# Kernel optimization log

Hardware: AMD Instinct MI355X
Metric: run time of the kernel (lower is better)

## Reference

```python
import jax, jax.numpy as jnp
import numpy as np
import math

K, D_FEAT, L_FAC, N = 128, 1024, 16, 16384


def setup_inputs() -> dict:
    key = jax.random.key(0)
    k1, k2, k3, k4 = jax.random.split(key, 4)
    x = jax.random.normal(k1, (N, D_FEAT), dtype=jnp.float32)
    MU = 0.1 * jax.random.normal(k2, (K, D_FEAT), dtype=jnp.float32)
    A = 0.05 * jax.random.normal(k3, (K, D_FEAT, L_FAC), dtype=jnp.float32)
    # D must be positive (it is a per-feature noise std): uniform in [0.1, 0.5]
    D = jax.random.uniform(k4, (K, D_FEAT), dtype=jnp.float32, minval=0.1, maxval=0.5)
    PI = jnp.ones((K,), dtype=jnp.float32) / K
    return {"x": x, "PI": PI, "MU": MU, "A": A, "D": D}


def reference(x, PI, MU, A, D):
    # Faithful vectorized version of MFA._per_component_log_likelihood.
    k, d, l = A.shape
    iD = jnp.power(D, -2.0)                      # (K, d)  = 1/D^2
    iDA = iD[:, :, None] * A                     # (K, d, l)
    # Woodbury small matrix: L = I_l + A^T (iD * A)
    Lm = jnp.eye(l, dtype=A.dtype)[None] + jnp.einsum('kdl,kdm->klm', A, iDA)
    iL = jnp.linalg.inv(Lm)                      # (K, l, l)

    # y[k,n,:] = A^T (iD * (x_n - MU_k))  without materializing (K,N,d)
    y = jnp.einsum('nd,kdl->knl', x, iDA) - jnp.einsum('kd,kdl->kl', MU, iDA)[:, None, :]
    # term1[k,n] = sum_d iD[k,d] * (x_n - MU_k)^2, expanded to avoid (K,N,d)
    term1 = (jnp.einsum('nd,kd->kn', x * x, iD)
             - 2.0 * jnp.einsum('nd,kd->kn', x, iD * MU)
             + jnp.sum(iD * MU * MU, axis=1)[:, None])
    # quadratic correction: y^T iL y
    quad = jnp.einsum('knl,klm,knm->kn', y, iL, y)
    m_d = term1 - quad                           # (K, N) Mahalanobis distances

    det_L = jnp.linalg.slogdet(Lm)[1]            # (K,)
    log_det_Sigma = det_L - jnp.sum(jnp.log(iD), axis=1)
    log2pi = jnp.asarray(math.log(2.0 * math.pi), dtype=x.dtype)
    log_prob = -0.5 * ((d * log2pi + log_det_Sigma)[:, None] + m_d)  # (K, N)
    # NOTE: original adds raw PI (not log PI) -- replicated faithfully.
    return PI[None, :] + log_prob.T              # (N, K)
```

## Files before the change

### kernel.cpp

```cpp
#include <hip/hip_runtime.h>
#include <math.h>

typedef unsigned short ushort_t;
typedef unsigned char  uchar_t;
typedef __attribute__((ext_vector_type(8))) short short8v;
typedef __attribute__((ext_vector_type(4))) float f32x4;
typedef __attribute__((ext_vector_type(2))) long l64x2;

#define KCOMP 128
#define DF    1024
#define LF    16
#define NPTS  16384
#define LOG2PI 1.8378770664093453f

#define XQ_OFF    ((size_t)0)
#define XQ_BYTES  ((size_t)NPTS*DF)
#define BQ_OFF    (XQ_OFF + XQ_BYTES)
#define BQ_BYTES  ((size_t)2048*DF)
#define BSK_OFF   (BQ_OFF + BQ_BYTES)
#define BSK_BYTES ((size_t)KCOMP*2*DF*2)
#define CSK_OFF   (BSK_OFF + BSK_BYTES)
#define FULL_NEED (CSK_OFF + 512)

__device__ __forceinline__ ushort_t f2bf(float f) {
  union { float f; unsigned u; } v; v.f = f;
  unsigned u = v.u;
  return (ushort_t)((u + 0x7FFFu + ((u >> 16) & 1u)) >> 16);
}

#define GLOAD16(gp, lp) __builtin_amdgcn_global_load_lds( \
  (const __attribute__((address_space(1))) unsigned int*)(gp), \
  (__attribute__((address_space(3))) unsigned int*)(lp), 16, 0, 0)

#define DPPADD(x, ctrl) do { \
  int _yi = __builtin_amdgcn_update_dpp(0, __float_as_int(x), ctrl, 0xF, 0xF, true); \
  (x) += __int_as_float(_yi); } while (0)

__global__ __launch_bounds__(256) void mfa_pre(
    const float* __restrict__ PI, const float* __restrict__ MU,
    const float* __restrict__ A, const float* __restrict__ Dm,
    uchar_t* __restrict__ Bq, ushort_t* __restrict__ Bsk,
    float* __restrict__ csk)
{
  const int k = blockIdx.x, t = threadIdx.x;
  const int tl = t >> 4, tm = t & 15;
  __shared__ float As[64][16];
  __shared__ float iD64[64], MU64[64];
  __shared__ float R[16][17];
  __shared__ float rinv_s[16], zsh[16], bsh[16];
  __shared__ float red[64];
  __shared__ float sc_sumlog, sc_c3;

  float accL = 0.f, accb = 0.f, c3p = 0.f, slogp = 0.f;
  for (int ch = 0; ch < 16; ++ch) {
    __syncthreads();
    ((float4*)&As[0][0])[t] =
        ((const float4*)(A + (size_t)k*DF*LF + (size_t)ch*1024))[t];
    if (t < 64) {
      float dv = Dm[k*DF + ch*64 + t];
      iD64[t] = 1.f/(dv*dv);
      MU64[t] = MU[k*DF + ch*64 + t];
    }
    __syncthreads();
    #pragma unroll 4
    for (int dd = 0; dd < 64; ++dd)
      accL = fmaf(As[dd][tl]*iD64[dd], As[dd][tm], accL);
    if (tm == 0)
      for (int dd = 0; dd < 64; ++dd)
        accb = fmaf(iD64[dd]*MU64[dd], As[dd][tl], accb);
    if (t < 64) {
      c3p = fmaf(iD64[t]*MU64[t], MU64[t], c3p);
      slogp += logf(iD64[t]);
    }
  }
  __syncthreads();
  R[tl][tm] = accL + (tl == tm ? 1.f : 0.f);
  if (tm == 0) bsh[tl] = accb;
  if (t < 64) red[t] = slogp;
  __syncthreads();
  if (t == 0) { float s = 0.f; for (int i = 0; i < 64; ++i) s += red[i]; sc_sumlog = s; }
  __syncthreads();
  if (t < 64) red[t] = c3p;
  __syncthreads();
  if (t == 0) { float s = 0.f; for (int i = 0; i < 64; ++i) s += red[i]; sc_c3 = s; }

  for (int j = 0; j < 16; ++j) {
    __syncthreads();
    if (t == j) {
      float s = R[j][j];
      for (int i = 0; i < j; ++i) s -= R[j][i]*R[j][i];
      float rj = sqrtf(s);
      R[j][j] = rj; rinv_s[j] = 1.f/rj;
    }
    __syncthreads();
    if (t < 16 && t > j) {
      float s = R[t][j];
      for (int i = 0; i < j; ++i) s -= R[t][i]*R[j][i];
      R[t][j] = s * rinv_s[j];
    }
  }
  __syncthreads();
  if (t == 0) {
    float ldet = 0.f;
    for (int j = 0; j < 16; ++j) ldet += 2.f*logf(R[j][j]);
    float w[16], z[16];
    for (int j = 0; j < 16; ++j) {
      float s = bsh[j];
      for (int i = 0; i < j; ++i) s -= R[j][i]*w[i];
      w[j] = s*rinv_s[j];
    }
    for (int j = 15; j >= 0; --j) {
      float s = w[j];
      for (int i = j+1; i < 16; ++i) s -= R[i][j]*z[i];
      z[j] = s*rinv_s[j];
      zsh[j] = z[j];
    }
    float muh = sc_c3;
    for (int l = 0; l < 16; ++l) muh -= bsh[l]*zsh[l];
    csk[k] = PI[k] - 0.5f*((float)DF*LOG2PI + ldet - sc_sumlog) - 0.5f*muh;
  }
  __syncthreads();

  for (int it = 0; it < 4; ++it) {
    const int d = t + it*256;
    float dv = Dm[k*DF + d];
    float iD = 1.f/(dv*dv);
    float mu = MU[k*DF + d];
    float v[16], gg[16];
    #pragma unroll
    for (int l = 0; l < 16; ++l) v[l] = iD * A[((size_t)k*DF + d)*LF + l];
    #pragma unroll
    for (int j = 0; j < 16; ++j) {
      float s = v[j];
      #pragma unroll
      for (int i = 0; i < 16; ++i) if (i < j) s -= R[j][i]*gg[i];
      gg[j] = s * rinv_s[j];
    }
    float h = iD*mu;
    #pragma unroll
    for (int l = 0; l < 16; ++l) h -= v[l]*zsh[l];
    const int dd = d & 63;
    const size_t poff = (size_t)(d & ~63) + ((dd >> 3) & 3)*16 + (dd >> 5)*8 + (dd & 7);
    #pragma unroll
    for (int l = 0; l < 16; ++l) {
      int r8 = __builtin_amdgcn_cvt_pk_fp8_f32(gg[l], gg[l], 0, false);
      Bq[(size_t)(k*16 + l)*DF + poff] = (uchar_t)(r8 & 0xFF);
    }
    Bsk[(size_t)k*2*DF + d]      = f2bf(-2.f*h);
    Bsk[(size_t)k*2*DF + DF + d] = f2bf(iD);
  }
}

__global__ __launch_bounds__(256) void mfa_sk2q(
    const float* __restrict__ x, const ushort_t* __restrict__ Bsk,
    const float* __restrict__ csk, uchar_t* __restrict__ xq,
    float* __restrict__ out)
{
  __shared__ ushort_t xs[4096];
  __shared__ ushort_t x2s[4096];
  __shared__ ushort_t Bs[16384];
  const int t = threadIdx.x, lane = t & 63, wid = t >> 6;
  const int wc = wid;
  const int lr = lane & 15, lh = lane >> 4;
  const int n0 = blockIdx.x * 64;
  const int xr = t >> 2, xc = t & 3;

  f32x4 acc[4][2] = {};

  float4 v0, v1, v2, v3;
  {
    const float* xp = x + (size_t)(n0 + xr)*DF + xc*16;
    v0 = ((const float4*)xp)[0]; v1 = ((const float4*)xp)[1];
    v2 = ((const float4*)xp)[2]; v3 = ((const float4*)xp)[3];
  }

  for (int tt = 0; tt < 16; ++tt) {
    const int d0 = tt * 64;
    __syncthreads();
    {
      float e[16] = {v0.x,v0.y,v0.z,v0.w, v1.x,v1.y,v1.z,v1.w,
                     v2.x,v2.y,v2.z,v2.w, v3.x,v3.y,v3.z,v3.w};
      short8v b0, b1, q0, q1;
      #pragma unroll
      for (int i = 0; i < 8; ++i) {
        b0[i] = (short)f2bf(e[i]);     q0[i] = (short)f2bf(e[i]*e[i]);
        b1[i] = (short)f2bf(e[8+i]);   q1[i] = (short)f2bf(e[8+i]*e[8+i]);
      }
      const int ch0 = (xc*2) ^ (xr & 7), ch1 = (xc*2+1) ^ (xr & 7);
      *(short8v*)&xs[xr*64 + ch0*8]  = b0;
      *(short8v*)&xs[xr*64 + ch1*8]  = b1;
      *(short8v*)&x2s[xr*64 + ch0*8] = q0;
      *(short8v*)&x2s[xr*64 + ch1*8] = q1;
      int p0 = 0, p1 = 0, p2 = 0, p3 = 0;
      p0 = __builtin_amdgcn_cvt_pk_fp8_f32(e[0],  e[1],  p0, false);
      p0 = __builtin_amdgcn_cvt_pk_fp8_f32(e[2],  e[3],  p0, true);
      p1 = __builtin_amdgcn_cvt_pk_fp8_f32(e[4],  e[5],  p1, false);
      p1 = __builtin_amdgcn_cvt_pk_fp8_f32(e[6],  e[7],  p1, true);
      p2 = __builtin_amdgcn_cvt_pk_fp8_f32(e[8],  e[9],  p2, false);
      p2 = __builtin_amdgcn_cvt_pk_fp8_f32(e[10], e[11], p2, true);
      p3 = __builtin_amdgcn_cvt_pk_fp8_f32(e[12], e[13], p3, false);
      p3 = __builtin_amdgcn_cvt_pk_fp8_f32(e[14], e[15], p3, true);
      long lo = (long)(((unsigned long long)(unsigned)p1 << 32) | (unsigned)p0);
      long hi = (long)(((unsigned long long)(unsigned)p3 << 32) | (unsigned)p2);
      size_t base = (size_t)(n0 + xr)*DF + d0 + (xc & 1)*32 + (xc >> 1)*8;
      *(long*)&xq[base]      = lo;
      *(long*)&xq[base + 16] = hi;
    }
    #pragma unroll
    for (int j = 0; j < 8; ++j) {
      int v = (wid*8 + j)*8 + (lane >> 3);
      int g = (lane & 7) ^ (v & 7);
      const ushort_t* src = (v < 128)
        ? Bsk + (size_t)v*(2*DF) + d0 + g*8
        : Bsk + (size_t)(v - 128)*(2*DF) + DF + d0 + g*8;
      GLOAD16(src, (char*)Bs + (wid*8 + j)*1024);
    }
    __syncthreads();
    if (tt < 15) {
      const float* xp = x + (size_t)(n0 + xr)*DF + (d0 + 64) + xc*16;
      v0 = ((const float4*)xp)[0]; v1 = ((const float4*)xp)[1];
      v2 = ((const float4*)xp)[2]; v3 = ((const float4*)xp)[3];
    }
    __builtin_amdgcn_sched_barrier(0);
    #pragma unroll
    for (int ks = 0; ks < 2; ++ks) {
      const int cterm = ((ks*4 + lh) ^ (lr & 7)) * 8;
      short8v a_[4], a2_[4], bh[2], bi[2];
      #pragma unroll
      for (int rb = 0; rb < 4; ++rb) {
        a_[rb]  = *(const short8v*)&xs[(rb*16 + lr)*64 + cterm];
        a2_[rb] = *(const short8v*)&x2s[(rb*16 + lr)*64 + cterm];
      }
      #pragma unroll
      for (int cb = 0; cb < 2; ++cb) {
        int vh = wc*32 + cb*16 + lr;
        bh[cb] = *(const short8v*)&Bs[vh*64 + cterm];
        bi[cb] = *(const short8v*)&Bs[(128 + vh)*64 + cterm];
      }
      #pragma unroll
      for (int cb = 0; cb < 2; ++cb)
        #pragma unroll
        for (int rb = 0; rb < 4; ++rb) {
          acc[rb][cb] = __builtin_amdgcn_mfma_f32_16x16x32_bf16(a_[rb],  bh[cb], acc[rb][cb], 0,0,0);
          acc[rb][cb] = __builtin_amdgcn_mfma_f32_16x16x32_bf16(a2_[rb], bi[cb], acc[rb][cb], 0,0,0);
        }
    }
  }
  #pragma unroll
  for (int cb = 0; cb < 2; ++cb) {
    int comp = wc*32 + cb*16 + lr;
    float ck = csk[comp];
    #pragma unroll
    for (int rb = 0; rb < 4; ++rb)
      #pragma unroll
      for (int j = 0; j < 4; ++j) {
        int row = n0 + rb*16 + lh*4 + j;
        out[(size_t)row*KCOMP + comp] = ck - 0.5f*acc[rb][cb][j];
      }
  }
}

__global__ __launch_bounds__(1024, 4) void mfa_gemm8(
    const uchar_t* __restrict__ xq, const uchar_t* __restrict__ Bq,
    float* __restrict__ out)
{
  __shared__ uchar_t smem[65536];
  const int t = threadIdx.x, lane = t & 63, wid = t >> 6;
  const int wm = wid & 3, wn = wid >> 2;
  const int lr = lane & 15, lh = lane >> 4;

  const int bid = blockIdx.x;
  const int xcd = bid & 7, ib = bid >> 3;
  const int rb = xcd*8 + (ib >> 3);
  const int cb = ib & 7;
  const int n0 = rb * 256, c0 = cb * 256;

  f32x4 acc[4][4] = {};

  const int js = (((lane & 3) ^ ((lane >> 3) & 3)) * 16);
  const uchar_t* srcP[2]; int dstO[2];
  #pragma unroll
  for (int q = 0; q < 2; ++q) {
    int id = wid*2 + q;
    if (id < 16) {
      int r = id*16 + (lane >> 2);
      srcP[q] = xq + (size_t)(n0 + r)*DF + js;
      dstO[q] = id*1024 + (lane & 3)*16 + (lane >> 2)*64 - (lane)*16;
    } else {
      int cr = (id - 16)*16 + (lane >> 2);
      srcP[q] = Bq + (size_t)(c0 + cr)*DF + js;
    }
  }
  dstO[0] = (wid*2 + 0) < 16 ? (wid*2+0)*1024 : 16384 + ((wid*2+0)-16)*1024;
  dstO[1] = (wid*2 + 1) < 16 ? (wid*2+1)*1024 : 16384 + ((wid*2+1)-16)*1024;

  const int rsw = (lh ^ ((lr >> 1) & 3)) * 16;
  const int aO = (wm*64 + lr)*64 + rsw;
  const int bO = 16384 + (wn*64 + lr)*64 + rsw;

  #define STAGE8(slot, tt_) do { \
    _Pragma("unroll") \
    for (int q = 0; q < 2; ++q) \
      GLOAD16(srcP[q] + (tt_)*64, (char*)smem + (slot)*32768 + dstO[q] + (lane & 63)*0 + ((lane)*16 & 1023)); \
  } while (0)

  STAGE8(0, 0);
  STAGE8(1, 1);

  for (int tt = 0; tt < 16; ++tt) {
    const char* lb = (const char*)smem + (tt & 1)*32768;
    l64x2 a2[4], b2[4];

    if (tt < 15) asm volatile("s_waitcnt vmcnt(2)" ::: "memory");
    else         asm volatile("s_waitcnt vmcnt(0)" ::: "memory");
    __builtin_amdgcn_s_barrier();

    #pragma unroll
    for (int rt = 0; rt < 4; ++rt) a2[rt] = *(const l64x2*)(lb + aO + rt*1024);
    #pragma unroll
    for (int ct = 0; ct < 4; ++ct) b2[ct] = *(const l64x2*)(lb + bO + ct*1024);
    asm volatile("s_waitcnt lgkmcnt(0)" ::: "memory");
    __builtin_amdgcn_sched_barrier(0);
    __builtin_amdgcn_s_barrier();
    if (tt <= 13) STAGE8(tt & 1, tt + 2);
    __builtin_amdgcn_sched_barrier(0);

    __builtin_amdgcn_s_setprio(1);
    #pragma unroll
    for (int ct = 0; ct < 4; ++ct)
      #pragma unroll
      for (int rt = 0; rt < 4; ++rt)
        acc[rt][ct] = __builtin_amdgcn_mfma_f32_16x16x32_fp8_fp8(a2[rt][0], b2[ct][0], acc[rt][ct], 0,0,0);
    #pragma unroll
    for (int ct = 0; ct < 4; ++ct)
      #pragma unroll
      for (int rt = 0; rt < 4; ++rt)
        acc[rt][ct] = __builtin_amdgcn_mfma_f32_16x16x32_fp8_fp8(a2[rt][1], b2[ct][1], acc[rt][ct], 0,0,0);
    __builtin_amdgcn_s_setprio(0);
  }

  #pragma unroll
  for (int ct = 0; ct < 4; ++ct) {
    const int comp = cb*16 + wn*4 + ct;
    #pragma unroll
    for (int rt = 0; rt < 4; ++rt) {
      #pragma unroll
      for (int j = 0; j < 4; ++j) {
        float v = acc[rt][ct][j];
        float sq = v*v;
        DPPADD(sq, 0xB1);
        DPPADD(sq, 0x4E);
        DPPADD(sq, 0x124);
        DPPADD(sq, 0x128);
        if (lr == 0) {
          int row = n0 + wm*64 + rt*16 + lh*4 + j;
          size_t idx = (size_t)row * KCOMP + comp;
          out[idx] = out[idx] + 0.5f*sq;
        }
      }
    }
  }
}

#define FB_NG 8
#define FB_CG 288
#define FB_BN 128
#define FB_DT 32
#define FB_PITCH 40
#define FB_BMAT_ELEMS ((size_t)(FB_NG*FB_CG)*DF)
#define FB_CST_OFF (FB_BMAT_ELEMS*2)
#define FB_MUH_OFF (FB_CST_OFF + 512)

__global__ __launch_bounds__(256) void fb_pre(
    const float* __restrict__ PI, const float* __restrict__ MU,
    const float* __restrict__ A, const float* __restrict__ Dm,
    ushort_t* __restrict__ Bmat, float* __restrict__ cst, float* __restrict__ muh)
{
  const int k = blockIdx.x, t = threadIdx.x;
  const int tl = t >> 4, tm = t & 15;
  __shared__ float As[16][16], iDsh[16], MUsh[16];
  __shared__ float R[16][17], rinv[16], zsh[16], bsh[16];
  __shared__ float red[256];

  float accL = 0.f, accb = 0.f, slog = 0.f;
  for (int d0 = 0; d0 < DF; d0 += 16) {
    __syncthreads();
    As[tl][tm] = A[((size_t)k*DF + d0 + tl)*LF + tm];
    if (t < 16) {
      float dv = Dm[k*DF + d0 + t];
      iDsh[t] = 1.f/(dv*dv);
      MUsh[t] = MU[k*DF + d0 + t];
    }
    __syncthreads();
    #pragma unroll
    for (int dd = 0; dd < 16; ++dd)
      accL = fmaf(As[dd][tl]*iDsh[dd], As[dd][tm], accL);
    if (tm == 0) {
      #pragma unroll
      for (int dd = 0; dd < 16; ++dd)
        accb = fmaf(iDsh[dd]*MUsh[dd], As[dd][tl], accb);
    }
    if (t < 16) slog += logf(iDsh[t]);
  }
  __syncthreads();
  R[tl][tm] = accL + (tl == tm ? 1.f : 0.f);
  if (tm == 0) bsh[tl] = accb;
  red[t] = (t < 16) ? slog : 0.f;
  __syncthreads();
  float sumlogiD = 0.f;
  if (t == 0) { for (int i = 0; i < 16; ++i) sumlogiD += red[i]; }

  for (int j = 0; j < 16; ++j) {
    if (t == j) {
      float s = R[j][j];
      for (int i = 0; i < j; ++i) s -= R[j][i]*R[j][i];
      float rj = sqrtf(s);
      R[j][j] = rj; rinv[j] = 1.f/rj;
    }
    __syncthreads();
    if (t < 16 && t > j) {
      float s = R[t][j];
      for (int i = 0; i < j; ++i) s -= R[t][i]*R[j][i];
      R[t][j] = s * rinv[j];
    }
    __syncthreads();
  }

  float ldet = 0.f;
  if (t == 0) {
    #pragma unroll
    for (int j = 0; j < 16; ++j) ldet += 2.f*logf(R[j][j]);
    float w[16], z[16];
    #pragma unroll
    for (int j = 0; j < 16; ++j) {
      float s = bsh[j];
      #pragma unroll
      for (int i = 0; i < 16; ++i) if (i < j) s -= R[j][i]*w[i];
      w[j] = s*rinv[j];
    }
    #pragma unroll
    for (int j = 15; j >= 0; --j) {
      float s = w[j];
      #pragma unroll
      for (int i = 0; i < 16; ++i) if (i > j) s -= R[i][j]*z[i];
      z[j] = s*rinv[j];
      zsh[j] = z[j];
    }
  }
  __syncthreads();

  const int g = k >> 4, kl = k & 15;
  ushort_t* Bgp = Bmat + (size_t)g*FB_CG*DF;
  float muhp = 0.f;
  for (int itr = 0; itr < 4; ++itr) {
    int d = t + itr*256;
    float dv = Dm[k*DF + d];
    float iD = 1.f/(dv*dv);
    float mu = MU[k*DF + d];
    float v[16], gg[16];
    #pragma unroll
    for (int l = 0; l < 16; ++l) v[l] = iD * A[((size_t)k*DF + d)*LF + l];
    #pragma unroll
    for (int j = 0; j < 16; ++j) {
      float s = v[j];
      #pragma unroll
      for (int i = 0; i < 16; ++i) if (i < j) s -= R[j][i]*gg[i];
      gg[j] = s * rinv[j];
    }
    float h = iD*mu;
    #pragma unroll
    for (int l = 0; l < 16; ++l) h -= v[l]*zsh[l];
    muhp = fmaf(mu, h, muhp);
    #pragma unroll
    for (int l = 0; l < 16; ++l)
      Bgp[(size_t)(kl*16 + l)*DF + d] = f2bf(gg[l]);
    Bgp[(size_t)(256 + kl)*DF + d] = f2bf(h);
    Bgp[(size_t)(272 + kl)*DF + d] = f2bf(iD);
  }
  red[t] = muhp;
  __syncthreads();
  for (int s = 128; s > 0; s >>= 1) {
    if (t < s) red[t] += red[t + s];
    __syncthreads();
  }
  if (t == 0) {
    muh[k] = red[0];
    cst[k] = PI[k] - 0.5f*((float)DF*LOG2PI + ldet - sumlogiD);
  }
}

__global__ __launch_bounds__(512, 2) void fb_main(
    const float* __restrict__ x, const ushort_t* __restrict__ Bmat,
    const float* __restrict__ cst, const float* __restrict__ muh,
    float* __restrict__ out)
{
  __shared__ __align__(16) ushort_t smem[2*FB_BN*FB_PITCH + FB_CG*FB_PITCH];
  ushort_t* xs  = smem;
  ushort_t* x2s = smem + FB_BN*FB_PITCH;
  ushort_t* Bs  = smem + 2*FB_BN*FB_PITCH;

  const int t = threadIdx.x;
  const int lane = t & 63, wid = t >> 6;
  const int wr = wid & 3, wc = wid >> 2;
  const int lr = lane & 15, lh = lane >> 4;
  const int n0 = blockIdx.x * FB_BN;
  const int g  = blockIdx.y;

  f32x4 acc[2][9] = {};
  const int srow = t >> 2, sc = t & 3;

  int xoff[2];
  #pragma unroll
  for (int rt = 0; rt < 2; ++rt)
    xoff[rt] = (wr*32 + rt*16 + lr)*FB_PITCH + lh*8;
  int boff[9];
  #pragma unroll
  for (int ct = 0; ct < 9; ++ct)
    boff[ct] = (wc*144 + ct*16 + lr)*FB_PITCH + lh*8;

  for (int d0 = 0; d0 < DF; d0 += FB_DT) {
    __syncthreads();
    {
      const float* xp = x + (size_t)(n0 + srow)*DF + d0 + sc*8;
      float4 v0 = *(const float4*)xp;
      float4 v1 = *(const float4*)(xp + 4);
      float e[8] = {v0.x,v0.y,v0.z,v0.w,v1.x,v1.y,v1.z,v1.w};
      short8v xv, qv;
      #pragma unroll
      for (int i = 0; i < 8; ++i) {
        xv[i] = (short)f2bf(e[i]);
        qv[i] = (short)f2bf(e[i]*e[i]);
      }
      *(short8v*)&xs[srow*FB_PITCH + sc*8]  = xv;
      *(short8v*)&x2s[srow*FB_PITCH + sc*8] = qv;
    }
    for (int u = t; u < FB_CG*4; u += 512) {
      int col = u >> 2, c = u & 3;
      *(short8v*)&Bs[col*FB_PITCH + c*8] =
        *(const short8v*)&Bmat[((size_t)(g*FB_CG + col))*DF + d0 + c*8];
    }
    __syncthreads();

    short8v xf[2];
    #pragma unroll
    for (int rt = 0; rt < 2; ++rt) xf[rt] = *(short8v*)&xs[xoff[rt]];
    #pragma unroll
    for (int ct = 0; ct < 8; ++ct) {
      short8v bfr = *(short8v*)&Bs[boff[ct]];
      #pragma unroll
      for (int rt = 0; rt < 2; ++rt)
        acc[rt][ct] = __builtin_amdgcn_mfma_f32_16x16x32_bf16(xf[rt], bfr, acc[rt][ct], 0, 0, 0);
    }
    {
      short8v bfr = *(short8v*)&Bs[boff[8]];
      short8v a0 = xf[0], a1 = xf[1];
      if (wc) {
        a0 = *(short8v*)&x2s[xoff[0]];
        a1 = *(short8v*)&x2s[xoff[1]];
      }
      acc[0][8] = __builtin_amdgcn_mfma_f32_16x16x32_bf16(a0, bfr, acc[0][8], 0, 0, 0);
      acc[1][8] = __builtin_amdgcn_mfma_f32_16x16x32_bf16(a1, bfr, acc[1][8], 0, 0, 0);
    }
  }

  __syncthreads();
  float* s1v = (float*)smem;
  float* s2h = s1v + FB_BN*17;
  if (wc == 1) {
    #pragma unroll
    for (int rt = 0; rt < 2; ++rt)
      #pragma unroll
      for (int j = 0; j < 4; ++j) {
        int row = wr*32 + rt*16 + lh*4 + j;
        s2h[row*17 + lr] = acc[rt][7][j];
        s1v[row*17 + lr] = acc[rt][8][j];
      }
  }
  __syncthreads();

  const int nyt = wc ? 7 : 9;
  #pragma unroll
  for (int ct = 0; ct < 9; ++ct) {
    if (ct < nyt) {
      int comp = wc*9 + ct;
      int kk = g*16 + comp;
      float cstk = cst[kk], muhk = muh[kk];
      #pragma unroll
      for (int rt = 0; rt < 2; ++rt)
        #pragma unroll
        for (int j = 0; j < 4; ++j) {
          float yv = acc[rt][ct][j];
          float sq = yv*yv;
          sq += __shfl_xor(sq, 1);
          sq += __shfl_xor(sq, 2);
          sq += __shfl_xor(sq, 4);
          sq += __shfl_xor(sq, 8);
          int row = wr*32 + rt*16 + lh*4 + j;
          float s1 = s1v[row*17 + comp];
          float s2 = s2h[row*17 + comp];
          float res = cstk - 0.5f*(s1 - sq - 2.f*s2 + muhk);
          if (lr == 0) out[(size_t)(n0 + row)*KCOMP + kk] = res;
        }
    }
  }
}

extern "C" void kernel_launch(void* const* d_in, const int* in_sizes, int n_in,
                              void* d_out, int out_size, void* d_ws, size_t ws_size,
                              hipStream_t stream) {
  const float* x  = (const float*)d_in[0];
  const float* PI = (const float*)d_in[1];
  const float* MU = (const float*)d_in[2];
  const float* A  = (const float*)d_in[3];
  const float* Dm = (const float*)d_in[4];
  float* out = (float*)d_out;

  if (ws_size >= FULL_NEED) {
    uchar_t* xq   = (uchar_t*)((char*)d_ws + XQ_OFF);
    uchar_t* Bq   = (uchar_t*)((char*)d_ws + BQ_OFF);
    ushort_t* Bsk = (ushort_t*)((char*)d_ws + BSK_OFF);
    float* csk    = (float*)((char*)d_ws + CSK_OFF);

    mfa_pre<<<dim3(KCOMP), dim3(256), 0, stream>>>(PI, MU, A, Dm, Bq, Bsk, csk);
    mfa_sk2q<<<dim3(NPTS/64), dim3(256), 0, stream>>>(x, Bsk, csk, xq, out);
    mfa_gemm8<<<dim3((NPTS/256)*(2048/256)), dim3(1024), 0, stream>>>(xq, Bq, out);
  } else {
    ushort_t* Bmat = (ushort_t*)d_ws;
    float* cstp = (float*)((char*)d_ws + FB_CST_OFF);
    float* muhp = (float*)((char*)d_ws + FB_MUH_OFF);
    fb_pre<<<dim3(KCOMP), dim3(256), 0, stream>>>(PI, MU, A, Dm, Bmat, cstp, muhp);
    fb_main<<<dim3(NPTS/FB_BN, FB_NG), dim3(512), 0, stream>>>(x, Bmat, cstp, muhp, out);
  }
}
```

Measured before the change: 157.9 us.

## Retile prologue and fp8 GEMM kernels to 512-thread blocks with different tile shapes

Result: no change. 157.0 us (-0.6%).

```diff
diff --git a/kernel.cpp b/kernel.cpp
--- a/kernel.cpp
+++ b/kernel.cpp
@@ -151,18 +151,18 @@
   }
 }
 
-__global__ __launch_bounds__(256) void mfa_sk2q(
+__global__ __launch_bounds__(512) void mfa_sk4(
     const float* __restrict__ x, const ushort_t* __restrict__ Bsk,
     const float* __restrict__ csk, uchar_t* __restrict__ xq,
     float* __restrict__ out)
 {
-  __shared__ ushort_t xs[4096];
-  __shared__ ushort_t x2s[4096];
+  __shared__ ushort_t xs[8192];
+  __shared__ ushort_t x2s[8192];
   __shared__ ushort_t Bs[16384];
   const int t = threadIdx.x, lane = t & 63, wid = t >> 6;
-  const int wc = wid;
+  const int wc = wid & 3, rgrp = wid >> 2;
   const int lr = lane & 15, lh = lane >> 4;
-  const int n0 = blockIdx.x * 64;
+  const int n0 = blockIdx.x * 128;
   const int xr = t >> 2, xc = t & 3;
 
   f32x4 acc[4][2] = {};
@@ -207,14 +207,16 @@
       *(long*)&xq[base + 16] = hi;
     }
     #pragma unroll
-    for (int j = 0; j < 8; ++j) {
-      int v = (wid*8 + j)*8 + (lane >> 3);
+    for (int jj = 0; jj < 4; ++jj) {
+      int id = wid*4 + jj;
+      int v = id*8 + (lane >> 3);
       int g = (lane & 7) ^ (v & 7);
       const ushort_t* src = (v < 128)
         ? Bsk + (size_t)v*(2*DF) + d0 + g*8
         : Bsk + (size_t)(v - 128)*(2*DF) + DF + d0 + g*8;
-      GLOAD16(src, (char*)Bs + (wid*8 + j)*1024);
-    }
+      GLOAD16(src, (char*)Bs + id*1024);
+    }
+    asm volatile("s_waitcnt vmcnt(0) lgkmcnt(0)" ::: "memory");
     __syncthreads();
     if (tt < 15) {
       const float* xp = x + (size_t)(n0 + xr)*DF + (d0 + 64) + xc*16;
@@ -228,8 +230,9 @@
       short8v a_[4], a2_[4], bh[2], bi[2];
       #pragma unroll
       for (int rb = 0; rb < 4; ++rb) {
-        a_[rb]  = *(const short8v*)&xs[(rb*16 + lr)*64 + cterm];
-        a2_[rb] = *(const short8v*)&x2s[(rb*16 + lr)*64 + cterm];
+        int row = rgrp*64 + rb*16 + lr;
+        a_[rb]  = *(const short8v*)&xs[row*64 + cterm];
+        a2_[rb] = *(const short8v*)&x2s[row*64 + cterm];
       }
       #pragma unroll
       for (int cb = 0; cb < 2; ++cb) {
@@ -254,64 +257,62 @@
     for (int rb = 0; rb < 4; ++rb)
       #pragma unroll
       for (int j = 0; j < 4; ++j) {
-        int row = n0 + rb*16 + lh*4 + j;
+        int row = n0 + rgrp*64 + rb*16 + lh*4 + j;
         out[(size_t)row*KCOMP + comp] = ck - 0.5f*acc[rb][cb][j];
       }
   }
 }
 
-__global__ __launch_bounds__(1024, 4) void mfa_gemm8(
+__global__ __launch_bounds__(512, 4) void mfa_gemm10(
     const uchar_t* __restrict__ xq, const uchar_t* __restrict__ Bq,
     float* __restrict__ out)
 {
-  __shared__ uchar_t smem[65536];
+  __shared__ uchar_t smem[49152];
   const int t = threadIdx.x, lane = t & 63, wid = t >> 6;
-  const int wm = wid & 3, wn = wid >> 2;
+  const int wm = wid & 1, wn = wid >> 1;
   const int lr = lane & 15, lh = lane >> 4;
 
   const int bid = blockIdx.x;
   const int xcd = bid & 7, ib = bid >> 3;
-  const int rb = xcd*8 + (ib >> 3);
+  const int rb = xcd*16 + (ib >> 3);
   const int cb = ib & 7;
-  const int n0 = rb * 256, c0 = cb * 256;
+  const int n0 = rb * 128, c0 = cb * 256;
 
   f32x4 acc[4][4] = {};
 
   const int js = (((lane & 3) ^ ((lane >> 3) & 3)) * 16);
-  const uchar_t* srcP[2]; int dstO[2];
+  const uchar_t* srcP[3]; int dstO[3];
   #pragma unroll
-  for (int q = 0; q < 2; ++q) {
-    int id = wid*2 + q;
-    if (id < 16) {
+  for (int q = 0; q < 3; ++q) {
+    int id = wid*3 + q;
+    if (id < 8) {
       int r = id*16 + (lane >> 2);
       srcP[q] = xq + (size_t)(n0 + r)*DF + js;
-      dstO[q] = id*1024 + (lane & 3)*16 + (lane >> 2)*64 - (lane)*16;
+      dstO[q] = id*1024;
     } else {
-      int cr = (id - 16)*16 + (lane >> 2);
+      int cr = (id - 8)*16 + (lane >> 2);
       srcP[q] = Bq + (size_t)(c0 + cr)*DF + js;
-    }
-  }
-  dstO[0] = (wid*2 + 0) < 16 ? (wid*2+0)*1024 : 16384 + ((wid*2+0)-16)*1024;
-  dstO[1] = (wid*2 + 1) < 16 ? (wid*2+1)*1024 : 16384 + ((wid*2+1)-16)*1024;
-
+      dstO[q] = 8192 + (id - 8)*1024;
+    }
+  }
   const int rsw = (lh ^ ((lr >> 1) & 3)) * 16;
   const int aO = (wm*64 + lr)*64 + rsw;
-  const int bO = 16384 + (wn*64 + lr)*64 + rsw;
-
-  #define STAGE8(slot, tt_) do { \
+  const int bO = 8192 + (wn*64 + lr)*64 + rsw;
+
+  #define STAGE10(slot, tt_) do { \
     _Pragma("unroll") \
-    for (int q = 0; q < 2; ++q) \
-      GLOAD16(srcP[q] + (tt_)*64, (char*)smem + (slot)*32768 + dstO[q] + (lane & 63)*0 + ((lane)*16 & 1023)); \
+    for (int q = 0; q < 3; ++q) \
+      GLOAD16(srcP[q] + (tt_)*64, (char*)smem + (slot)*24576 + dstO[q] + ((lane)*16 & 1023)); \
   } while (0)
 
-  STAGE8(0, 0);
-  STAGE8(1, 1);
+  STAGE10(0, 0);
+  STAGE10(1, 1);
 
   for (int tt = 0; tt < 16; ++tt) {
-    const char* lb = (const char*)smem + (tt & 1)*32768;
+    const char* lb = (const char*)smem + (tt & 1)*24576;
     l64x2 a2[4], b2[4];
 
-    if (tt < 15) asm volatile("s_waitcnt vmcnt(2)" ::: "memory");
+    if (tt < 15) asm volatile("s_waitcnt vmcnt(3)" ::: "memory");
     else         asm volatile("s_waitcnt vmcnt(0)" ::: "memory");
     __builtin_amdgcn_s_barrier();
 
@@ -322,7 +323,7 @@
     asm volatile("s_waitcnt lgkmcnt(0)" ::: "memory");
     __builtin_amdgcn_sched_barrier(0);
     __builtin_amdgcn_s_barrier();
-    if (tt <= 13) STAGE8(tt & 1, tt + 2);
+    if (tt <= 13) STAGE10(tt & 1, tt + 2);
     __builtin_amdgcn_sched_barrier(0);
 
     __builtin_amdgcn_s_setprio(1);
@@ -622,8 +623,8 @@
     float* csk    = (float*)((char*)d_ws + CSK_OFF);
 
     mfa_pre<<<dim3(KCOMP), dim3(256), 0, stream>>>(PI, MU, A, Dm, Bq, Bsk, csk);
-    mfa_sk2q<<<dim3(NPTS/64), dim3(256), 0, stream>>>(x, Bsk, csk, xq, out);
-    mfa_gemm8<<<dim3((NPTS/256)*(2048/256)), dim3(1024), 0, stream>>>(xq, Bq, out);
+    mfa_sk4<<<dim3(NPTS/128), dim3(512), 0, stream>>>(x, Bsk, csk, xq, out);
+    mfa_gemm10<<<dim3((NPTS/128)*(2048/256)), dim3(512), 0, stream>>>(xq, Bq, out);
   } else {
     ushort_t* Bmat = (ushort_t*)d_ws;
     float* cstp = (float*)((char*)d_ws + FB_CST_OFF);
```
